# Kernel tuning notes

Hardware: AMD Instinct MI355X
Metric: run time of the kernel (lower is better)

Reference implementation:

```python
import jax, jax.numpy as jnp
import numpy as np

N = 8192
E = 262144
C = 256          # in_channels
OUT = 256        # out_channels
H = 4            # num_heads
DH = C // H      # head dim


def setup_inputs() -> dict:
    key = jax.random.key(0)
    ks = jax.random.split(key, 12)
    stdv = 1.0 / np.sqrt(C)
    inp = {
        "x": jax.random.normal(ks[0], (N, C), dtype=jnp.float32),
        "adj": jax.random.randint(ks[1], (2, E), 0, N, dtype=jnp.int64),
        "weight_local": jax.random.uniform(ks[2], (C, C), jnp.float32, -stdv, stdv),
        # nn.MultiheadAttention packed projections
        "in_proj_w": jax.random.normal(ks[3], (3 * C, C), jnp.float32) * stdv,
        "in_proj_b": jnp.zeros((3 * C,), jnp.float32),
        "out_proj_w": jax.random.normal(ks[4], (C, C), jnp.float32) * stdv,
        "out_proj_b": jnp.zeros((C,), jnp.float32),
        "ln_g": jnp.ones((C,), jnp.float32),
        "ln_b": jnp.zeros((C,), jnp.float32),
        "alpha": jnp.zeros((), jnp.float32),
        "fc_w": jax.random.normal(ks[5], (OUT, C), jnp.float32) * stdv,
        "fc_b": jnp.zeros((OUT,), jnp.float32),
    }
    return inp


def _gcn_conv(x, edge_index):
    # out[col] += (1/sqrt(d[col]*d[row])) * x[row], d = in-degree by col
    row, col = edge_index[0], edge_index[1]
    n = x.shape[0]
    d = jax.ops.segment_sum(jnp.ones((edge_index.shape[1],), x.dtype), col, num_segments=n)
    val = jax.lax.rsqrt(d[col] * d[row])
    val = jnp.where(jnp.isfinite(val), val, 0.0)
    msg = x[row] * val[:, None]                      # [E, C] gather + scale
    return jax.ops.segment_sum(msg, col, num_segments=n)  # [N, C] scatter-add


def _mha(x, in_proj_w, in_proj_b, out_proj_w, out_proj_b):
    # single-batch self-attention over all N nodes
    qkv = x @ in_proj_w.T + in_proj_b                # [N, 3C]
    q, k, v = jnp.split(qkv, 3, axis=-1)
    def heads(t):
        return t.reshape(N, H, DH).transpose(1, 0, 2)  # [H, N, DH]
    q, k, v = heads(q), heads(k), heads(v)
    scores = jnp.einsum("hnd,hmd->hnm", q, k) / np.sqrt(DH)  # [H, N, N]
    attn = jax.nn.softmax(scores, axis=-1)
    out = jnp.einsum("hnm,hmd->hnd", attn, v)        # [H, N, DH]
    out = out.transpose(1, 0, 2).reshape(N, C)
    return out @ out_proj_w.T + out_proj_b


def _layernorm(x, g, b, eps=1e-5):
    mu = jnp.mean(x, axis=-1, keepdims=True)
    var = jnp.var(x, axis=-1, keepdims=True)
    return (x - mu) * jax.lax.rsqrt(var + eps) * g + b


def reference(x, adj, weight_local, in_proj_w, in_proj_b, out_proj_w, out_proj_b,
              ln_g, ln_b, alpha, fc_w, fc_b):
    hi = _gcn_conv(x, adj)
    local_embed = hi @ weight_local                   # [N, C]
    attn_out = _mha(x, in_proj_w, in_proj_b, out_proj_w, out_proj_b)
    global_embed = _layernorm(x + attn_out, ln_g, ln_b)
    w = jax.nn.sigmoid(alpha)
    combined = w * local_embed + (1.0 - w) * global_embed
    return combined @ fc_w.T + fc_b                   # [N, OUT]
```

## Files before the change

kernel.cpp:

```cpp
#include <hip/hip_runtime.h>
#include <hip/hip_bf16.h>
#include <math.h>

#define NN   8192
#define EE   262144
#define CC   256
#define HH   4

typedef __bf16 bf16;
typedef __bf16 bf16x8 __attribute__((ext_vector_type(8)));
typedef __bf16 bf16x4 __attribute__((ext_vector_type(4)));
typedef __bf16 bf16x2 __attribute__((ext_vector_type(2)));
typedef float  f32x4  __attribute__((ext_vector_type(4)));

static __device__ __forceinline__ bf16 f2bf(float f) { return (bf16)f; }

static __device__ __forceinline__ unsigned pk2(float a, float b) {
    __hip_bfloat162 h = __float22bfloat162_rn(float2{a, b});
    return *reinterpret_cast<unsigned*>(&h);
}

__global__ void cvt_f32_bf16(const float* __restrict__ in, bf16* __restrict__ out, int n) {
    for (int i = blockIdx.x * blockDim.x + threadIdx.x; i < n; i += gridDim.x * blockDim.x)
        out[i] = f2bf(in[i]);
}

__global__ void cvt_weights(const float* __restrict__ ipw, const float* __restrict__ opw,
                            const float* __restrict__ fcw, const float* __restrict__ wloc,
                            bf16* __restrict__ ipwb, bf16* __restrict__ opwb,
                            bf16* __restrict__ fcwb, bf16* __restrict__ wlTb) {
    int b = blockIdx.x, t = threadIdx.x;
    if (b < 768)       { int i = b * 256 + t;          ipwb[i] = f2bf(ipw[i]); }
    else if (b < 1024) { int i = (b - 768) * 256 + t;  opwb[i] = f2bf(opw[i]); }
    else if (b < 1280) { int i = (b - 1024) * 256 + t; fcwb[i] = f2bf(fcw[i]); }
    else               { int n = b - 1280;             wlTb[n * 256 + t] = f2bf(wloc[t * 256 + n]); }
}

__global__ __launch_bounds__(256) void build_kpk(const bf16* __restrict__ qkv,
                                                 bf16* __restrict__ Kpk) {
    __shared__ bf16 tl[64][72];
    const int bx = blockIdx.x;
    const int h  = blockIdx.y;
    const int tid = threadIdx.x;
    #pragma unroll
    for (int i = 0; i < 2; i++) {
        int u = tid + i * 256;
        int key = u >> 3, g = u & 7;
        *reinterpret_cast<bf16x8*>(&tl[key][g * 8]) =
            *reinterpret_cast<const bf16x8*>(qkv + (size_t)(bx * 64 + key) * 768 + 256 + h * 64 + g * 8);
    }
    __syncthreads();
    #pragma unroll
    for (int i = 0; i < 2; i++) {
        int ee = tid + i * 256;
        int l15 = ee & 15, quad = (ee >> 4) & 3, c = (ee >> 6) & 1, ktl = ee >> 7;
        int key_local = (ktl >> 1) * 32 + (l15 >> 2) * 8 + (ktl & 1) * 4 + (l15 & 3);
        bf16x8 v = *reinterpret_cast<const bf16x8*>(&tl[key_local][c * 32 + quad * 8]);
        *reinterpret_cast<bf16x8*>(Kpk + ((size_t)((h * 512 + bx * 4 + ktl) * 2 + c)) * 512
                                       + (quad * 16 + l15) * 8) = v;
    }
}

__global__ __launch_bounds__(256) void build_vpk(const bf16* __restrict__ qkv,
                                                 bf16* __restrict__ Vpk) {
    __shared__ bf16 tl[64][72];
    const int bx = blockIdx.x;
    const int h  = blockIdx.y;
    const int tid = threadIdx.x;
    #pragma unroll
    for (int i = 0; i < 2; i++) {
        int u = tid + i * 256;
        int key = u >> 3, g = u & 7;
        *reinterpret_cast<bf16x8*>(&tl[key][g * 8]) =
            *reinterpret_cast<const bf16x8*>(qkv + (size_t)(bx * 64 + key) * 768 + 512 + h * 64 + g * 8);
    }
    __syncthreads();
    #pragma unroll
    for (int i = 0; i < 2; i++) {
        int ee = tid + i * 256;
        int l15 = ee & 15, quad = (ee >> 4) & 3, nt = (ee >> 6) & 3, kcl = ee >> 8;
        bf16x8 v;
        #pragma unroll
        for (int j = 0; j < 8; j++) v[j] = tl[kcl * 32 + quad * 8 + j][nt * 16 + l15];
        *reinterpret_cast<bf16x8*>(Vpk + ((size_t)((h * 256 + bx * 2 + kcl) * 4 + nt)) * 512
                                       + (quad * 16 + l15) * 8) = v;
    }
}

__global__ void degree_i(const int* __restrict__ adj, int* __restrict__ ideg) {
    int e = blockIdx.x * 256 + threadIdx.x;
    if (e < EE) atomicAdd(&ideg[adj[EE + e]], 1);
}

__global__ __launch_bounds__(256) void scan_offsets(const int* __restrict__ ideg,
        int* __restrict__ off, int* __restrict__ cursor, float* __restrict__ rs) {
    __shared__ int ps[256];
    const int tid = threadIdx.x;
    const int base = tid * 32;
    int loc[32];
    int s = 0;
    #pragma unroll
    for (int i = 0; i < 32; i++) { loc[i] = s; s += ideg[base + i]; }
    ps[tid] = s;
    __syncthreads();
    for (int d = 1; d < 256; d <<= 1) {
        int v = (tid >= d) ? ps[tid - d] : 0;
        __syncthreads();
        ps[tid] += v;
        __syncthreads();
    }
    int excl = ps[tid] - s;
    #pragma unroll
    for (int i = 0; i < 32; i++) {
        int o = excl + loc[i];
        off[base + i] = o;
        cursor[base + i] = o;
        int dg = ideg[base + i];
        rs[base + i] = dg > 0 ? rsqrtf((float)dg) : 0.f;
    }
    if (tid == 255) off[8192] = excl + s;
}

__global__ void fill_csr(const int* __restrict__ adj, int* __restrict__ cursor,
                         int* __restrict__ csr) {
    int e = blockIdx.x * 256 + threadIdx.x;
    if (e < EE) {
        int col = adj[EE + e];
        int pos = atomicAdd(&cursor[col], 1);
        csr[pos] = adj[e];
    }
}

__global__ __launch_bounds__(256) void gcn_gather2(const bf16* __restrict__ xb,
        const int* __restrict__ csr, const int* __restrict__ off,
        const float* __restrict__ rs, bf16* __restrict__ hib) {
    const int col = blockIdx.x;
    const int t = threadIdx.x;
    const int half = t >> 7;
    const int j = t & 127;
    const int o = off[col];
    const int cnt = off[col + 1] - o;
    const float rsc = rs[col];
    float a0 = 0.f, a1 = 0.f;
    for (int e = half; e < cnt; e += 2) {
        int r = csr[o + e];
        float v = rsc * rs[r];
        unsigned u = ((const unsigned*)(xb + (size_t)r * CC))[j];
        a0 += __uint_as_float(u << 16) * v;
        a1 += __uint_as_float(u & 0xffff0000u) * v;
    }
    __shared__ float red[512];
    red[half * 256 + 2 * j]     = a0;
    red[half * 256 + 2 * j + 1] = a1;
    __syncthreads();
    if (t < 128) {
        float s0 = red[2 * t]     + red[256 + 2 * t];
        float s1 = red[2 * t + 1] + red[256 + 2 * t + 1];
        bf16x2 pk; pk[0] = f2bf(s0); pk[1] = f2bf(s1);
        ((bf16x2*)(hib + (size_t)col * CC))[t] = pk;
    }
}

__global__ __launch_bounds__(256) void gemm_bt(
        const bf16* __restrict__ A, const bf16* __restrict__ W,
        const float* __restrict__ bias,
        float* __restrict__ outF, bf16* __restrict__ outB,
        int M, int N, int K) {
    const int tid  = threadIdx.x;
    const int wave = tid >> 6;
    const int lane = tid & 63;
    const int quad = lane >> 4;
    const int l15  = lane & 15;
    const int m0 = blockIdx.x * 128;
    const int n0 = blockIdx.y * 64;

    __shared__ bf16 Alds[128][72];
    __shared__ bf16 Wlds[64][72];

    f32x4 acc[2][4];
    #pragma unroll
    for (int mt = 0; mt < 2; mt++)
        #pragma unroll
        for (int nt = 0; nt < 4; nt++)
            acc[mt][nt] = (f32x4){0.f, 0.f, 0.f, 0.f};

    for (int k0 = 0; k0 < K; k0 += 64) {
        #pragma unroll
        for (int i = 0; i < 4; i++) {
            int u = tid + i * 256;
            int r = u >> 3;
            int cp = u & 7;
            *reinterpret_cast<bf16x8*>(&Alds[r][cp * 8]) =
                *reinterpret_cast<const bf16x8*>(A + (size_t)(m0 + r) * K + k0 + cp * 8);
        }
        #pragma unroll
        for (int i = 0; i < 2; i++) {
            int u = tid + i * 256;
            int r = u >> 3;
            int cp = u & 7;
            *reinterpret_cast<bf16x8*>(&Wlds[r][cp * 8]) =
                *reinterpret_cast<const bf16x8*>(W + (size_t)(n0 + r) * K + k0 + cp * 8);
        }
        __syncthreads();
        #pragma unroll
        for (int c = 0; c < 2; c++) {
            bf16x8 af[2], wf[4];
            #pragma unroll
            for (int mt = 0; mt < 2; mt++)
                af[mt] = *reinterpret_cast<const bf16x8*>(&Alds[wave * 32 + mt * 16 + l15][c * 32 + quad * 8]);
            #pragma unroll
            for (int nt = 0; nt < 4; nt++)
                wf[nt] = *reinterpret_cast<const bf16x8*>(&Wlds[nt * 16 + l15][c * 32 + quad * 8]);
            #pragma unroll
            for (int mt = 0; mt < 2; mt++)
                #pragma unroll
                for (int nt = 0; nt < 4; nt++)
                    acc[mt][nt] = __builtin_amdgcn_mfma_f32_16x16x32_bf16(af[mt], wf[nt], acc[mt][nt], 0, 0, 0);
        }
        __syncthreads();
    }
    #pragma unroll
    for (int mt = 0; mt < 2; mt++)
        #pragma unroll
        for (int nt = 0; nt < 4; nt++)
            #pragma unroll
            for (int r = 0; r < 4; r++) {
                int m = m0 + wave * 32 + mt * 16 + quad * 4 + r;
                int n = n0 + nt * 16 + l15;
                float v = acc[mt][nt][r];
                if (bias) v += bias[n];
                if (outF) outF[(size_t)m * N + n] = v;
                else      outB[(size_t)m * N + n] = f2bf(v);
            }
}

__global__ __launch_bounds__(256, 2) void flash_attn6(const bf16* __restrict__ qkv,
                                                      const bf16* __restrict__ Kpk,
                                                      const bf16* __restrict__ Vpk,
                                                      bf16* __restrict__ attnO) {
    const int tid  = threadIdx.x;
    const int w    = tid >> 6;
    const int lane = tid & 63;
    const int quad = lane >> 4;
    const int l15  = lane & 15;
    const int h     = blockIdx.x & 3;
    const int qbase = (blockIdx.x >> 2) * 64;

    __shared__ bf16 Osh[4][64][68];
    __shared__ float lsh[4][64];

    const float qs = 0.180336880f;
    bf16x8 qf[4][2];
    #pragma unroll
    for (int qt = 0; qt < 4; qt++)
        #pragma unroll
        for (int c = 0; c < 2; c++) {
            bf16x8 raw = *reinterpret_cast<const bf16x8*>(
                qkv + (size_t)(qbase + qt * 16 + l15) * 768 + h * 64 + c * 32 + quad * 8);
            #pragma unroll
            for (int j = 0; j < 8; j++) qf[qt][c][j] = f2bf((float)raw[j] * qs);
        }

    const bf16* Kb = Kpk + (size_t)h * 524288 + lane * 8;
    const bf16* Vb = Vpk + (size_t)h * 524288 + lane * 8;

    f32x4 oacc[4][4];
    #pragma unroll
    for (int qt = 0; qt < 4; qt++)
        #pragma unroll
        for (int nt = 0; nt < 4; nt++) oacc[qt][nt] = (f32x4){0.f, 0.f, 0.f, 0.f};
    f32x4 lacc[4];
    #pragma unroll
    for (int qt = 0; qt < 4; qt++) lacc[qt] = (f32x4){0.f, 0.f, 0.f, 0.f};
    bf16x8 onesf;
    #pragma unroll
    for (int j = 0; j < 8; j++) onesf[j] = f2bf(1.0f);
    const f32x4 z4 = (f32x4){0.f, 0.f, 0.f, 0.f};

    bf16x8 kfA[2][2], vfA[4], kfB[2][2], vfB[4];

    #define LOADKV(kc, kf, vf)                                                          \
        {                                                                               \
            _Pragma("unroll")                                                           \
            for (int s = 0; s < 2; s++)                                                 \
                _Pragma("unroll")                                                       \
                for (int c = 0; c < 2; c++)                                             \
                    kf[s][c] = *reinterpret_cast<const bf16x8*>(Kb + (kc) * 2048 + s * 1024 + c * 512); \
            _Pragma("unroll")                                                           \
            for (int nt = 0; nt < 4; nt++)                                              \
                vf[nt] = *reinterpret_cast<const bf16x8*>(Vb + (kc) * 2048 + nt * 512); \
        }

    #define COMPUTE(kf, vf)                                                             \
        {                                                                               \
            f32x4 sacc[2][4];                                                           \
            _Pragma("unroll")                                                           \
            for (int s = 0; s < 2; s++)                                                 \
                _Pragma("unroll")                                                       \
                for (int qt = 0; qt < 4; qt++) {                                        \
                    sacc[s][qt] = __builtin_amdgcn_mfma_f32_16x16x32_bf16(kf[s][0], qf[qt][0], z4, 0, 0, 0); \
                    sacc[s][qt] = __builtin_amdgcn_mfma_f32_16x16x32_bf16(kf[s][1], qf[qt][1], sacc[s][qt], 0, 0, 0); \
                }                                                                       \
            _Pragma("unroll")                                                           \
            for (int qt = 0; qt < 4; qt++) {                                            \
                float e0 = __builtin_amdgcn_exp2f(sacc[0][qt][0]);                      \
                float e1 = __builtin_amdgcn_exp2f(sacc[0][qt][1]);                      \
                float e2 = __builtin_amdgcn_exp2f(sacc[0][qt][2]);                      \
                float e3 = __builtin_amdgcn_exp2f(sacc[0][qt][3]);                      \
                float e4 = __builtin_amdgcn_exp2f(sacc[1][qt][0]);                      \
                float e5 = __builtin_amdgcn_exp2f(sacc[1][qt][1]);                      \
                float e6 = __builtin_amdgcn_exp2f(sacc[1][qt][2]);                      \
                float e7 = __builtin_amdgcn_exp2f(sacc[1][qt][3]);                      \
                union { bf16x8 v; unsigned u[4]; } pu;                                  \
                pu.u[0] = pk2(e0, e1);                                                  \
                pu.u[1] = pk2(e2, e3);                                                  \
                pu.u[2] = pk2(e4, e5);                                                  \
                pu.u[3] = pk2(e6, e7);                                                  \
                _Pragma("unroll")                                                       \
                for (int nt = 0; nt < 4; nt++)                                          \
                    oacc[qt][nt] = __builtin_amdgcn_mfma_f32_16x16x32_bf16(pu.v, vf[nt], oacc[qt][nt], 0, 0, 0); \
                lacc[qt] = __builtin_amdgcn_mfma_f32_16x16x32_bf16(pu.v, onesf, lacc[qt], 0, 0, 0); \
            }                                                                           \
        }

    LOADKV(w, kfA, vfA);
    for (int it = 0; it < 64; it += 2) {
        const int kB = w + (it + 1) * 4;
        LOADKV(kB, kfB, vfB);
        COMPUTE(kfA, vfA);
        int kA2 = w + (it + 2) * 4;
        if (kA2 > 255) kA2 = w;
        LOADKV(kA2, kfA, vfA);
        COMPUTE(kfB, vfB);
    }
    #undef LOADKV
    #undef COMPUTE

    #pragma unroll
    for (int qt = 0; qt < 4; qt++)
        #pragma unroll
        for (int nt = 0; nt < 4; nt++)
            #pragma unroll
            for (int r = 0; r < 4; r++)
                Osh[w][qt * 16 + quad * 4 + r][nt * 16 + l15] = f2bf(oacc[qt][nt][r]);
    if (l15 == 0) {
        #pragma unroll
        for (int qt = 0; qt < 4; qt++)
            #pragma unroll
            for (int r = 0; r < 4; r++)
                lsh[w][qt * 16 + quad * 4 + r] = lacc[qt][r];
    }
    __syncthreads();

    const int q = w * 16 + l15;
    float lstar = lsh[0][q] + lsh[1][q] + lsh[2][q] + lsh[3][q];
    float linv = 1.f / lstar;
    #pragma unroll
    for (int gg = 0; gg < 4; gg++) {
        int d0 = gg * 16 + quad * 4;
        f32x4 acc = (f32x4){0.f, 0.f, 0.f, 0.f};
        #pragma unroll
        for (int v = 0; v < 4; v++) {
            bf16x4 ov = *reinterpret_cast<const bf16x4*>(&Osh[v][q][d0]);
            #pragma unroll
            for (int i = 0; i < 4; i++) acc[i] += (float)ov[i];
        }
        bf16x4 ob;
        #pragma unroll
        for (int i = 0; i < 4; i++) ob[i] = f2bf(acc[i] * linv);
        *reinterpret_cast<bf16x4*>(attnO + (size_t)(qbase + q) * CC + h * 64 + d0) = ob;
    }
}

__global__ __launch_bounds__(256) void ln_combine2(
        const float* __restrict__ x, const float* __restrict__ aproj,
        const float* __restrict__ local, const float* __restrict__ g,
        const float* __restrict__ b, const float* __restrict__ alpha_p,
        bf16* __restrict__ comb) {
    const int row = blockIdx.x * 4 + (threadIdx.x >> 6);
    const int lane = threadIdx.x & 63;
    const f32x4 xv = ((const f32x4*)(x + (size_t)row * CC))[lane];
    const f32x4 av = ((const f32x4*)(aproj + (size_t)row * CC))[lane];
    f32x4 v = xv + av;
    float s = v[0] + v[1] + v[2] + v[3];
    #pragma unroll
    for (int off = 1; off < 64; off <<= 1) s += __shfl_xor(s, off);
    float mu = s * (1.f / CC);
    f32x4 d = v - mu;
    float ss = d[0] * d[0] + d[1] * d[1] + d[2] * d[2] + d[3] * d[3];
    #pragma unroll
    for (int off = 1; off < 64; off <<= 1) ss += __shfl_xor(ss, off);
    float rstd = rsqrtf(ss * (1.f / CC) + 1e-5f);
    const f32x4 gv = ((const f32x4*)g)[lane];
    const f32x4 bv = ((const f32x4*)b)[lane];
    const f32x4 lv = ((const f32x4*)(local + (size_t)row * CC))[lane];
    float wgt = 1.f / (1.f + __expf(-alpha_p[0]));
    bf16x4 o;
    #pragma unroll
    for (int i = 0; i < 4; i++)
        o[i] = f2bf(wgt * lv[i] + (1.f - wgt) * (d[i] * rstd * gv[i] + bv[i]));
    ((bf16x4*)(comb + (size_t)row * CC))[lane] = o;
}

extern "C" void kernel_launch(void* const* d_in, const int* in_sizes, int n_in,
                              void* d_out, int out_size, void* d_ws, size_t ws_size,
                              hipStream_t stream) {
    (void)in_sizes; (void)n_in; (void)out_size; (void)ws_size;
    const float* x    = (const float*)d_in[0];
    const int*   adj  = (const int*)d_in[1];
    const float* wloc = (const float*)d_in[2];
    const float* ipw  = (const float*)d_in[3];
    const float* ipb  = (const float*)d_in[4];
    const float* opw  = (const float*)d_in[5];
    const float* opb  = (const float*)d_in[6];
    const float* lng  = (const float*)d_in[7];
    const float* lnb  = (const float*)d_in[8];
    const float* alp  = (const float*)d_in[9];
    const float* fcw  = (const float*)d_in[10];
    const float* fcb  = (const float*)d_in[11];
    float* out = (float*)d_out;

    char* p = (char*)d_ws;
    int*   ideg   = (int*)p;    p += (size_t)NN * 4;
    int*   off    = (int*)p;    p += (size_t)(NN + 1) * 4;
    int*   cursor = (int*)p;    p += (size_t)NN * 4;
    float* rs     = (float*)p;  p += (size_t)NN * 4;
    int*   csr    = (int*)p;    p += (size_t)EE * 4;
    bf16* xb    = (bf16*)p;   p += (size_t)NN * CC * 2;
    bf16* hib   = (bf16*)p;   p += (size_t)NN * CC * 2;
    bf16* ipwb  = (bf16*)p;   p += (size_t)768 * 256 * 2;
    bf16* wlTb  = (bf16*)p;   p += (size_t)256 * 256 * 2;
    bf16* opwb  = (bf16*)p;   p += (size_t)256 * 256 * 2;
    bf16* fcwb  = (bf16*)p;   p += (size_t)256 * 256 * 2;
    bf16* qkvb  = (bf16*)p;   p += (size_t)NN * 768 * 2;
    bf16* Kpk   = (bf16*)p;   p += (size_t)HH * 512 * 2 * 512 * 2;
    bf16* Vpk   = (bf16*)p;   p += (size_t)HH * 256 * 4 * 512 * 2;
    bf16* aOb   = (bf16*)p;   p += (size_t)NN * CC * 2;
    float* aprj = (float*)p;  p += (size_t)NN * CC * 4;
    float* locl = (float*)p;  p += (size_t)NN * CC * 4;
    bf16* comb  = (bf16*)p;   p += (size_t)NN * CC * 2;

    hipMemsetAsync(ideg, 0, (size_t)NN * 4, stream);

    cvt_f32_bf16<<<2048, 256, 0, stream>>>(x, xb, NN * CC);
    cvt_weights<<<1536, 256, 0, stream>>>(ipw, opw, fcw, wloc, ipwb, opwb, fcwb, wlTb);

    degree_i<<<EE / 256, 256, 0, stream>>>(adj, ideg);
    scan_offsets<<<1, 256, 0, stream>>>(ideg, off, cursor, rs);
    fill_csr<<<EE / 256, 256, 0, stream>>>(adj, cursor, csr);
    gcn_gather2<<<NN, 256, 0, stream>>>(xb, csr, off, rs, hib);

    gemm_bt<<<dim3(NN / 128, 768 / 64), 256, 0, stream>>>(xb, ipwb, ipb, nullptr, qkvb, NN, 768, 256);
    build_kpk<<<dim3(NN / 64, HH), 256, 0, stream>>>(qkvb, Kpk);
    build_vpk<<<dim3(NN / 64, HH), 256, 0, stream>>>(qkvb, Vpk);
    flash_attn6<<<512, 256, 0, stream>>>(qkvb, Kpk, Vpk, aOb);
    gemm_bt<<<dim3(NN / 128, 256 / 64), 256, 0, stream>>>(aOb, opwb, opb, aprj, nullptr, NN, 256, 256);
    gemm_bt<<<dim3(NN / 128, 256 / 64), 256, 0, stream>>>(hib, wlTb, nullptr, locl, nullptr, NN, 256, 256);
    ln_combine2<<<NN / 4, 256, 0, stream>>>(x, aprj, locl, lng, lnb, alp, comb);
    gemm_bt<<<dim3(NN / 128, 256 / 64), 256, 0, stream>>>(comb, fcwb, fcb, out, nullptr, NN, 256, 256);
}
```

Measured before the change: 297.8 us.

## Split attention keys across two blocks, merge partials, and fuse prep kernels

```diff
diff --git a/kernel.cpp b/kernel.cpp
--- a/kernel.cpp
+++ b/kernel.cpp
@@ -20,24 +20,28 @@
     return *reinterpret_cast<unsigned*>(&h);
 }
 
-__global__ void cvt_f32_bf16(const float* __restrict__ in, bf16* __restrict__ out, int n) {
-    for (int i = blockIdx.x * blockDim.x + threadIdx.x; i < n; i += gridDim.x * blockDim.x)
-        out[i] = f2bf(in[i]);
-}
-
-__global__ void cvt_weights(const float* __restrict__ ipw, const float* __restrict__ opw,
-                            const float* __restrict__ fcw, const float* __restrict__ wloc,
-                            bf16* __restrict__ ipwb, bf16* __restrict__ opwb,
-                            bf16* __restrict__ fcwb, bf16* __restrict__ wlTb) {
+__global__ void prep_all(const float* __restrict__ x, bf16* __restrict__ xb,
+                         const float* __restrict__ ipw, const float* __restrict__ opw,
+                         const float* __restrict__ fcw, const float* __restrict__ wloc,
+                         bf16* __restrict__ ipwb, bf16* __restrict__ opwb,
+                         bf16* __restrict__ fcwb, bf16* __restrict__ wlTb,
+                         const int* __restrict__ adj, int* __restrict__ ideg) {
     int b = blockIdx.x, t = threadIdx.x;
-    if (b < 768)       { int i = b * 256 + t;          ipwb[i] = f2bf(ipw[i]); }
-    else if (b < 1024) { int i = (b - 768) * 256 + t;  opwb[i] = f2bf(opw[i]); }
-    else if (b < 1280) { int i = (b - 1024) * 256 + t; fcwb[i] = f2bf(fcw[i]); }
-    else               { int n = b - 1280;             wlTb[n * 256 + t] = f2bf(wloc[t * 256 + n]); }
-}
-
-__global__ __launch_bounds__(256) void build_kpk(const bf16* __restrict__ qkv,
-                                                 bf16* __restrict__ Kpk) {
+    if (b < 2048) {
+        for (int i = b * 256 + t; i < NN * CC; i += 2048 * 256) xb[i] = f2bf(x[i]);
+    } else if (b < 2816) { int i = (b - 2048) * 256 + t; ipwb[i] = f2bf(ipw[i]); }
+    else if (b < 3072)   { int i = (b - 2816) * 256 + t; opwb[i] = f2bf(opw[i]); }
+    else if (b < 3328)   { int i = (b - 3072) * 256 + t; fcwb[i] = f2bf(fcw[i]); }
+    else if (b < 3584)   { int n = b - 3328;             wlTb[n * 256 + t] = f2bf(wloc[t * 256 + n]); }
+    else {
+        int e = (b - 3584) * 256 + t;
+        if (e < EE) atomicAdd(&ideg[adj[EE + e]], 1);
+    }
+}
+
+__global__ __launch_bounds__(256) void build_kv(const bf16* __restrict__ qkv,
+                                                bf16* __restrict__ Kpk,
+                                                bf16* __restrict__ Vpk) {
     __shared__ bf16 tl[64][72];
     const int bx = blockIdx.x;
     const int h  = blockIdx.y;
@@ -59,14 +63,7 @@
         *reinterpret_cast<bf16x8*>(Kpk + ((size_t)((h * 512 + bx * 4 + ktl) * 2 + c)) * 512
                                        + (quad * 16 + l15) * 8) = v;
     }
-}
-
-__global__ __launch_bounds__(256) void build_vpk(const bf16* __restrict__ qkv,
-                                                 bf16* __restrict__ Vpk) {
-    __shared__ bf16 tl[64][72];
-    const int bx = blockIdx.x;
-    const int h  = blockIdx.y;
-    const int tid = threadIdx.x;
+    __syncthreads();
     #pragma unroll
     for (int i = 0; i < 2; i++) {
         int u = tid + i * 256;
@@ -85,11 +82,6 @@
         *reinterpret_cast<bf16x8*>(Vpk + ((size_t)((h * 256 + bx * 2 + kcl) * 4 + nt)) * 512
                                        + (quad * 16 + l15) * 8) = v;
     }
-}
-
-__global__ void degree_i(const int* __restrict__ adj, int* __restrict__ ideg) {
-    int e = blockIdx.x * 256 + threadIdx.x;
-    if (e < EE) atomicAdd(&ideg[adj[EE + e]], 1);
 }
 
 __global__ __launch_bounds__(256) void scan_offsets(const int* __restrict__ ideg,
@@ -234,17 +226,21 @@
             }
 }
 
-__global__ __launch_bounds__(256, 2) void flash_attn6(const bf16* __restrict__ qkv,
+__global__ __launch_bounds__(256, 3) void flash_attn7(const bf16* __restrict__ qkv,
                                                       const bf16* __restrict__ Kpk,
                                                       const bf16* __restrict__ Vpk,
-                                                      bf16* __restrict__ attnO) {
+                                                      bf16* __restrict__ Opart,
+                                                      float* __restrict__ lpart) {
     const int tid  = threadIdx.x;
     const int w    = tid >> 6;
     const int lane = tid & 63;
     const int quad = lane >> 4;
     const int l15  = lane & 15;
-    const int h     = blockIdx.x & 3;
-    const int qbase = (blockIdx.x >> 2) * 64;
+    const int bx = blockIdx.x;
+    const int h    = bx & 3;
+    const int qb   = (bx >> 2) & 127;
+    const int half = bx >> 9;
+    const int qbase = qb * 64;
 
     __shared__ bf16 Osh[4][64][68];
     __shared__ float lsh[4][64];
@@ -263,6 +259,7 @@
 
     const bf16* Kb = Kpk + (size_t)h * 524288 + lane * 8;
     const bf16* Vb = Vpk + (size_t)h * 524288 + lane * 8;
+    const int cbase = half * 128 + w;
 
     f32x4 oacc[4][4];
     #pragma unroll
@@ -277,64 +274,47 @@
     for (int j = 0; j < 8; j++) onesf[j] = f2bf(1.0f);
     const f32x4 z4 = (f32x4){0.f, 0.f, 0.f, 0.f};
 
-    bf16x8 kfA[2][2], vfA[4], kfB[2][2], vfB[4];
-
-    #define LOADKV(kc, kf, vf)                                                          \
-        {                                                                               \
-            _Pragma("unroll")                                                           \
-            for (int s = 0; s < 2; s++)                                                 \
-                _Pragma("unroll")                                                       \
-                for (int c = 0; c < 2; c++)                                             \
-                    kf[s][c] = *reinterpret_cast<const bf16x8*>(Kb + (kc) * 2048 + s * 1024 + c * 512); \
-            _Pragma("unroll")                                                           \
-            for (int nt = 0; nt < 4; nt++)                                              \
-                vf[nt] = *reinterpret_cast<const bf16x8*>(Vb + (kc) * 2048 + nt * 512); \
-        }
-
-    #define COMPUTE(kf, vf)                                                             \
-        {                                                                               \
-            f32x4 sacc[2][4];                                                           \
-            _Pragma("unroll")                                                           \
-            for (int s = 0; s < 2; s++)                                                 \
-                _Pragma("unroll")                                                       \
-                for (int qt = 0; qt < 4; qt++) {                                        \
-                    sacc[s][qt] = __builtin_amdgcn_mfma_f32_16x16x32_bf16(kf[s][0], qf[qt][0], z4, 0, 0, 0); \
-                    sacc[s][qt] = __builtin_amdgcn_mfma_f32_16x16x32_bf16(kf[s][1], qf[qt][1], sacc[s][qt], 0, 0, 0); \
-                }                                                                       \
-            _Pragma("unroll")                                                           \
-            for (int qt = 0; qt < 4; qt++) {                                            \
-                float e0 = __builtin_amdgcn_exp2f(sacc[0][qt][0]);                      \
-                float e1 = __builtin_amdgcn_exp2f(sacc[0][qt][1]);                      \
-                float e2 = __builtin_amdgcn_exp2f(sacc[0][qt][2]);                      \
-                float e3 = __builtin_amdgcn_exp2f(sacc[0][qt][3]);                      \
-                float e4 = __builtin_amdgcn_exp2f(sacc[1][qt][0]);                      \
-                float e5 = __builtin_amdgcn_exp2f(sacc[1][qt][1]);                      \
-                float e6 = __builtin_amdgcn_exp2f(sacc[1][qt][2]);                      \
-                float e7 = __builtin_amdgcn_exp2f(sacc[1][qt][3]);                      \
-                union { bf16x8 v; unsigned u[4]; } pu;                                  \
-                pu.u[0] = pk2(e0, e1);                                                  \
-                pu.u[1] = pk2(e2, e3);                                                  \
-                pu.u[2] = pk2(e4, e5);                                                  \
-                pu.u[3] = pk2(e6, e7);                                                  \
-                _Pragma("unroll")                                                       \
-                for (int nt = 0; nt < 4; nt++)                                          \
-                    oacc[qt][nt] = __builtin_amdgcn_mfma_f32_16x16x32_bf16(pu.v, vf[nt], oacc[qt][nt], 0, 0, 0); \
-                lacc[qt] = __builtin_amdgcn_mfma_f32_16x16x32_bf16(pu.v, onesf, lacc[qt], 0, 0, 0); \
-            }                                                                           \
-        }
-
-    LOADKV(w, kfA, vfA);
-    for (int it = 0; it < 64; it += 2) {
-        const int kB = w + (it + 1) * 4;
-        LOADKV(kB, kfB, vfB);
-        COMPUTE(kfA, vfA);
-        int kA2 = w + (it + 2) * 4;
-        if (kA2 > 255) kA2 = w;
-        LOADKV(kA2, kfA, vfA);
-        COMPUTE(kfB, vfB);
-    }
-    #undef LOADKV
-    #undef COMPUTE
+    for (int i = 0; i < 32; i++) {
+        const int kc = cbase + i * 4;
+        bf16x8 kf[2][2], vf[4];
+        #pragma unroll
+        for (int s = 0; s < 2; s++)
+            #pragma unroll
+            for (int c = 0; c < 2; c++)
+                kf[s][c] = *reinterpret_cast<const bf16x8*>(Kb + kc * 2048 + s * 1024 + c * 512);
+        #pragma unroll
+        for (int nt = 0; nt < 4; nt++)
+            vf[nt] = *reinterpret_cast<const bf16x8*>(Vb + kc * 2048 + nt * 512);
+
+        f32x4 sacc[2][4];
+        #pragma unroll
+        for (int s = 0; s < 2; s++)
+            #pragma unroll
+            for (int qt = 0; qt < 4; qt++) {
+                sacc[s][qt] = __builtin_amdgcn_mfma_f32_16x16x32_bf16(kf[s][0], qf[qt][0], z4, 0, 0, 0);
+                sacc[s][qt] = __builtin_amdgcn_mfma_f32_16x16x32_bf16(kf[s][1], qf[qt][1], sacc[s][qt], 0, 0, 0);
+            }
+        #pragma unroll
+        for (int qt = 0; qt < 4; qt++) {
+            float e0 = __builtin_amdgcn_exp2f(sacc[0][qt][0]);
+            float e1 = __builtin_amdgcn_exp2f(sacc[0][qt][1]);
+            float e2 = __builtin_amdgcn_exp2f(sacc[0][qt][2]);
+            float e3 = __builtin_amdgcn_exp2f(sacc[0][qt][3]);
+            float e4 = __builtin_amdgcn_exp2f(sacc[1][qt][0]);
+            float e5 = __builtin_amdgcn_exp2f(sacc[1][qt][1]);
+            float e6 = __builtin_amdgcn_exp2f(sacc[1][qt][2]);
+            float e7 = __builtin_amdgcn_exp2f(sacc[1][qt][3]);
+            union { bf16x8 v; unsigned u[4]; } pu;
+            pu.u[0] = pk2(e0, e1);
+            pu.u[1] = pk2(e2, e3);
+            pu.u[2] = pk2(e4, e5);
+            pu.u[3] = pk2(e6, e7);
+            #pragma unroll
+            for (int nt = 0; nt < 4; nt++)
+                oacc[qt][nt] = __builtin_amdgcn_mfma_f32_16x16x32_bf16(pu.v, vf[nt], oacc[qt][nt], 0, 0, 0);
+            lacc[qt] = __builtin_amdgcn_mfma_f32_16x16x32_bf16(pu.v, onesf, lacc[qt], 0, 0, 0);
+        }
+    }
 
     #pragma unroll
     for (int qt = 0; qt < 4; qt++)
@@ -353,8 +333,10 @@
     __syncthreads();
 
     const int q = w * 16 + l15;
-    float lstar = lsh[0][q] + lsh[1][q] + lsh[2][q] + lsh[3][q];
-    float linv = 1.f / lstar;
+    const size_t ob = (size_t)half * 2097152 + ((size_t)(h * 128 + qb) * 64 + q) * 64;
+    if (quad == 0)
+        lpart[half * 32768 + (h * 128 + qb) * 64 + q] =
+            lsh[0][q] + lsh[1][q] + lsh[2][q] + lsh[3][q];
     #pragma unroll
     for (int gg = 0; gg < 4; gg++) {
         int d0 = gg * 16 + quad * 4;
@@ -365,11 +347,38 @@
             #pragma unroll
             for (int i = 0; i < 4; i++) acc[i] += (float)ov[i];
         }
-        bf16x4 ob;
-        #pragma unroll
-        for (int i = 0; i < 4; i++) ob[i] = f2bf(acc[i] * linv);
-        *reinterpret_cast<bf16x4*>(attnO + (size_t)(qbase + q) * CC + h * 64 + d0) = ob;
-    }
+        bf16x4 obv;
+        #pragma unroll
+        for (int i = 0; i < 4; i++) obv[i] = f2bf(acc[i]);
+        *reinterpret_cast<bf16x4*>(Opart + ob + d0) = obv;
+    }
+}
+
+__global__ __launch_bounds__(256) void attn_merge(const bf16* __restrict__ Opart,
+                                                  const float* __restrict__ lpart,
+                                                  bf16* __restrict__ attnO) {
+    const int b = blockIdx.x;
+    const int h = b >> 7;
+    const int qb = b & 127;
+    const int t = threadIdx.x;
+    const int q = t >> 2;
+    const int dg = t & 3;
+    const float linv = 1.f / (lpart[b * 64 + q] + lpart[32768 + b * 64 + q]);
+    const bf16* p0 = Opart + ((size_t)b * 64 + q) * 64 + dg * 16;
+    const bf16* p1 = p0 + 2097152;
+    bf16x8 a0 = *reinterpret_cast<const bf16x8*>(p0);
+    bf16x8 a1 = *reinterpret_cast<const bf16x8*>(p0 + 8);
+    bf16x8 b0 = *reinterpret_cast<const bf16x8*>(p1);
+    bf16x8 b1 = *reinterpret_cast<const bf16x8*>(p1 + 8);
+    bf16x8 o0, o1;
+    #pragma unroll
+    for (int i = 0; i < 8; i++) {
+        o0[i] = f2bf(((float)a0[i] + (float)b0[i]) * linv);
+        o1[i] = f2bf(((float)a1[i] + (float)b1[i]) * linv);
+    }
+    bf16* dst = attnO + (size_t)(qb * 64 + q) * CC + h * 64 + dg * 16;
+    *reinterpret_cast<bf16x8*>(dst) = o0;
+    *reinterpret_cast<bf16x8*>(dst + 8) = o1;
 }
 
 __global__ __launch_bounds__(256) void ln_combine2(
@@ -439,21 +448,20 @@
     float* aprj = (float*)p;  p += (size_t)NN * CC * 4;
     float* locl = (float*)p;  p += (size_t)NN * CC * 4;
     bf16* comb  = (bf16*)p;   p += (size_t)NN * CC * 2;
+    bf16*  Opart = (bf16*)aprj;
+    float* lpart = (float*)locl;
 
     hipMemsetAsync(ideg, 0, (size_t)NN * 4, stream);
 
-    cvt_f32_bf16<<<2048, 256, 0, stream>>>(x, xb, NN * CC);
-    cvt_weights<<<1536, 256, 0, stream>>>(ipw, opw, fcw, wloc, ipwb, opwb, fcwb, wlTb);
-
-    degree_i<<<EE / 256, 256, 0, stream>>>(adj, ideg);
+    prep_all<<<4608, 256, 0, stream>>>(x, xb, ipw, opw, fcw, wloc, ipwb, opwb, fcwb, wlTb, adj, ideg);
     scan_offsets<<<1, 256, 0, stream>>>(ideg, off, cursor, rs);
     fill_csr<<<EE / 256, 256, 0, stream>>>(adj, cursor, csr);
     gcn_gather2<<<NN, 256, 0, stream>>>(xb, csr, off, rs, hib);
 
     gemm_bt<<<dim3(NN / 128, 768 / 64), 256, 0, stream>>>(xb, ipwb, ipb, nullptr, qkvb, NN, 768, 256);
-    build_kpk<<<dim3(NN / 64, HH), 256, 0, stream>>>(qkvb, Kpk);
-    build_vpk<<<dim3(NN / 64, HH), 256, 0, stream>>>(qkvb, Vpk);
-    flash_attn6<<<512, 256, 0, stream>>>(qkvb, Kpk, Vpk, aOb);
+    build_kv<<<dim3(NN / 64, HH), 256, 0, stream>>>(qkvb, Kpk, Vpk);
+    flash_attn7<<<1024, 256, 0, stream>>>(qkvb, Kpk, Vpk, Opart, lpart);
+    attn_merge<<<512, 256, 0, stream>>>(Opart, lpart, aOb);
     gemm_bt<<<dim3(NN / 128, 256 / 64), 256, 0, stream>>>(aOb, opwb, opb, aprj, nullptr, NN, 256, 256);
     gemm_bt<<<dim3(NN / 128, 256 / 64), 256, 0, stream>>>(hib, wlTb, nullptr, locl, nullptr, NN, 256, 256);
     ln_combine2<<<NN / 4, 256, 0, stream>>>(x, aprj, locl, lng, lnb, alp, comb);
```

Result: slower. 310.0 us (+4.1%).

## Fuse prep and K/V packing kernels, merge GEMMs, widen flash-attention blocks

Applied to the files above, without the earlier changes.

```diff
diff --git a/kernel.cpp b/kernel.cpp
--- a/kernel.cpp
+++ b/kernel.cpp
@@ -20,24 +20,28 @@
     return *reinterpret_cast<unsigned*>(&h);
 }
 
-__global__ void cvt_f32_bf16(const float* __restrict__ in, bf16* __restrict__ out, int n) {
-    for (int i = blockIdx.x * blockDim.x + threadIdx.x; i < n; i += gridDim.x * blockDim.x)
-        out[i] = f2bf(in[i]);
-}
-
-__global__ void cvt_weights(const float* __restrict__ ipw, const float* __restrict__ opw,
-                            const float* __restrict__ fcw, const float* __restrict__ wloc,
-                            bf16* __restrict__ ipwb, bf16* __restrict__ opwb,
-                            bf16* __restrict__ fcwb, bf16* __restrict__ wlTb) {
+__global__ void prep_all(const float* __restrict__ x, bf16* __restrict__ xb,
+                         const float* __restrict__ ipw, const float* __restrict__ opw,
+                         const float* __restrict__ fcw, const float* __restrict__ wloc,
+                         bf16* __restrict__ ipwb, bf16* __restrict__ opwb,
+                         bf16* __restrict__ fcwb, bf16* __restrict__ wlTb,
+                         const int* __restrict__ adj, int* __restrict__ ideg) {
     int b = blockIdx.x, t = threadIdx.x;
-    if (b < 768)       { int i = b * 256 + t;          ipwb[i] = f2bf(ipw[i]); }
-    else if (b < 1024) { int i = (b - 768) * 256 + t;  opwb[i] = f2bf(opw[i]); }
-    else if (b < 1280) { int i = (b - 1024) * 256 + t; fcwb[i] = f2bf(fcw[i]); }
-    else               { int n = b - 1280;             wlTb[n * 256 + t] = f2bf(wloc[t * 256 + n]); }
-}
-
-__global__ __launch_bounds__(256) void build_kpk(const bf16* __restrict__ qkv,
-                                                 bf16* __restrict__ Kpk) {
+    if (b < 2048) {
+        for (int i = b * 256 + t; i < NN * CC; i += 2048 * 256) xb[i] = f2bf(x[i]);
+    } else if (b < 2816) { int i = (b - 2048) * 256 + t; ipwb[i] = f2bf(ipw[i]); }
+    else if (b < 3072)   { int i = (b - 2816) * 256 + t; opwb[i] = f2bf(opw[i]); }
+    else if (b < 3328)   { int i = (b - 3072) * 256 + t; fcwb[i] = f2bf(fcw[i]); }
+    else if (b < 3584)   { int n = b - 3328;             wlTb[n * 256 + t] = f2bf(wloc[t * 256 + n]); }
+    else {
+        int e = (b - 3584) * 256 + t;
+        if (e < EE) atomicAdd(&ideg[adj[EE + e]], 1);
+    }
+}
+
+__global__ __launch_bounds__(256) void build_kv(const bf16* __restrict__ qkv,
+                                                bf16* __restrict__ Kpk,
+                                                bf16* __restrict__ Vpk) {
     __shared__ bf16 tl[64][72];
     const int bx = blockIdx.x;
     const int h  = blockIdx.y;
@@ -59,14 +63,7 @@
         *reinterpret_cast<bf16x8*>(Kpk + ((size_t)((h * 512 + bx * 4 + ktl) * 2 + c)) * 512
                                        + (quad * 16 + l15) * 8) = v;
     }
-}
-
-__global__ __launch_bounds__(256) void build_vpk(const bf16* __restrict__ qkv,
-                                                 bf16* __restrict__ Vpk) {
-    __shared__ bf16 tl[64][72];
-    const int bx = blockIdx.x;
-    const int h  = blockIdx.y;
-    const int tid = threadIdx.x;
+    __syncthreads();
     #pragma unroll
     for (int i = 0; i < 2; i++) {
         int u = tid + i * 256;
@@ -85,11 +82,6 @@
         *reinterpret_cast<bf16x8*>(Vpk + ((size_t)((h * 256 + bx * 2 + kcl) * 4 + nt)) * 512
                                        + (quad * 16 + l15) * 8) = v;
     }
-}
-
-__global__ void degree_i(const int* __restrict__ adj, int* __restrict__ ideg) {
-    int e = blockIdx.x * 256 + threadIdx.x;
-    if (e < EE) atomicAdd(&ideg[adj[EE + e]], 1);
 }
 
 __global__ __launch_bounds__(256) void scan_offsets(const int* __restrict__ ideg,
@@ -161,11 +153,11 @@
     }
 }
 
-__global__ __launch_bounds__(256) void gemm_bt(
+static __device__ __forceinline__ void gemm_core(
         const bf16* __restrict__ A, const bf16* __restrict__ W,
         const float* __restrict__ bias,
         float* __restrict__ outF, bf16* __restrict__ outB,
-        int M, int N, int K) {
+        int M, int N, int K, bf16 (*Alds)[72], bf16 (*Wlds)[72]) {
     const int tid  = threadIdx.x;
     const int wave = tid >> 6;
     const int lane = tid & 63;
@@ -173,9 +165,6 @@
     const int l15  = lane & 15;
     const int m0 = blockIdx.x * 128;
     const int n0 = blockIdx.y * 64;
-
-    __shared__ bf16 Alds[128][72];
-    __shared__ bf16 Wlds[64][72];
 
     f32x4 acc[2][4];
     #pragma unroll
@@ -234,20 +223,45 @@
             }
 }
 
-__global__ __launch_bounds__(256, 2) void flash_attn6(const bf16* __restrict__ qkv,
-                                                      const bf16* __restrict__ Kpk,
-                                                      const bf16* __restrict__ Vpk,
-                                                      bf16* __restrict__ attnO) {
+__global__ __launch_bounds__(256) void gemm_bt(
+        const bf16* __restrict__ A, const bf16* __restrict__ W,
+        const float* __restrict__ bias,
+        float* __restrict__ outF, bf16* __restrict__ outB,
+        int M, int N, int K) {
+    __shared__ bf16 Alds[128][72];
+    __shared__ bf16 Wlds[64][72];
+    gemm_core(A, W, bias, outF, outB, M, N, K, Alds, Wlds);
+}
+
+__global__ __launch_bounds__(256) void gemm_dual(
+        const bf16* __restrict__ A0, const bf16* __restrict__ W0,
+        const float* __restrict__ b0, float* __restrict__ o0,
+        const bf16* __restrict__ A1, const bf16* __restrict__ W1,
+        float* __restrict__ o1) {
+    __shared__ bf16 Alds[128][72];
+    __shared__ bf16 Wlds[64][72];
+    if (blockIdx.z == 0) gemm_core(A0, W0, b0, o0, nullptr, NN, 256, 256, Alds, Wlds);
+    else                 gemm_core(A1, W1, nullptr, o1, nullptr, NN, 256, 256, Alds, Wlds);
+}
+
+__global__ __launch_bounds__(512, 2) void flash_attn10(const bf16* __restrict__ qkv,
+                                                       const bf16* __restrict__ Kpk,
+                                                       const bf16* __restrict__ Vpk,
+                                                       bf16* __restrict__ attnO) {
     const int tid  = threadIdx.x;
     const int w    = tid >> 6;
+    const int g    = w >> 2;
+    const int k4   = w & 3;
     const int lane = tid & 63;
     const int quad = lane >> 4;
     const int l15  = lane & 15;
-    const int h     = blockIdx.x & 3;
-    const int qbase = (blockIdx.x >> 2) * 64;
-
-    __shared__ bf16 Osh[4][64][68];
-    __shared__ float lsh[4][64];
+    const int bx = blockIdx.x;
+    const int h  = bx & 3;
+    const int qb = bx >> 2;
+    const int qbase = qb * 128 + g * 64;
+
+    __shared__ bf16 Osh[8][64][68];
+    __shared__ float lsh[8][64];
 
     const float qs = 0.180336880f;
     bf16x8 qf[4][2];
@@ -323,13 +337,13 @@
             }                                                                           \
         }
 
-    LOADKV(w, kfA, vfA);
+    LOADKV(k4, kfA, vfA);
     for (int it = 0; it < 64; it += 2) {
-        const int kB = w + (it + 1) * 4;
+        const int kB = k4 + (it + 1) * 4;
         LOADKV(kB, kfB, vfB);
         COMPUTE(kfA, vfA);
-        int kA2 = w + (it + 2) * 4;
-        if (kA2 > 255) kA2 = w;
+        int kA2 = k4 + (it + 2) * 4;
+        if (kA2 > 255) kA2 = k4;
         LOADKV(kA2, kfA, vfA);
         COMPUTE(kfB, vfB);
     }
@@ -352,24 +366,32 @@
     }
     __syncthreads();
 
-    const int q = w * 16 + l15;
-    float lstar = lsh[0][q] + lsh[1][q] + lsh[2][q] + lsh[3][q];
-    float linv = 1.f / lstar;
-    #pragma unroll
-    for (int gg = 0; gg < 4; gg++) {
-        int d0 = gg * 16 + quad * 4;
-        f32x4 acc = (f32x4){0.f, 0.f, 0.f, 0.f};
-        #pragma unroll
-        for (int v = 0; v < 4; v++) {
-            bf16x4 ov = *reinterpret_cast<const bf16x4*>(&Osh[v][q][d0]);
-            #pragma unroll
-            for (int i = 0; i < 4; i++) acc[i] += (float)ov[i];
-        }
-        bf16x4 ob;
-        #pragma unroll
-        for (int i = 0; i < 4; i++) ob[i] = f2bf(acc[i] * linv);
-        *reinterpret_cast<bf16x4*>(attnO + (size_t)(qbase + q) * CC + h * 64 + d0) = ob;
-    }
+    const int q7 = tid >> 2;
+    const int gg = q7 >> 6;
+    const int ql = q7 & 63;
+    const int ds = (tid & 3) * 16;
+    const int wb = gg * 4;
+    float lsum = lsh[wb][ql] + lsh[wb + 1][ql] + lsh[wb + 2][ql] + lsh[wb + 3][ql];
+    float linv = 1.f / lsum;
+    float acc[16];
+    #pragma unroll
+    for (int i = 0; i < 16; i++) acc[i] = 0.f;
+    #pragma unroll
+    for (int v = 0; v < 4; v++) {
+        bf16x8 o0 = *reinterpret_cast<const bf16x8*>(&Osh[wb + v][ql][ds]);
+        bf16x8 o1 = *reinterpret_cast<const bf16x8*>(&Osh[wb + v][ql][ds + 8]);
+        #pragma unroll
+        for (int i = 0; i < 8; i++) { acc[i] += (float)o0[i]; acc[8 + i] += (float)o1[i]; }
+    }
+    bf16x8 ob0, ob1;
+    #pragma unroll
+    for (int i = 0; i < 8; i++) {
+        ob0[i] = f2bf(acc[i] * linv);
+        ob1[i] = f2bf(acc[8 + i] * linv);
+    }
+    bf16* dst = attnO + (size_t)(qb * 128 + q7) * CC + h * 64 + ds;
+    *reinterpret_cast<bf16x8*>(dst) = ob0;
+    *reinterpret_cast<bf16x8*>(dst + 8) = ob1;
 }
 
 __global__ __launch_bounds__(256) void ln_combine2(
@@ -442,20 +464,15 @@
 
     hipMemsetAsync(ideg, 0, (size_t)NN * 4, stream);
 
-    cvt_f32_bf16<<<2048, 256, 0, stream>>>(x, xb, NN * CC);
-    cvt_weights<<<1536, 256, 0, stream>>>(ipw, opw, fcw, wloc, ipwb, opwb, fcwb, wlTb);
-
-    degree_i<<<EE / 256, 256, 0, stream>>>(adj, ideg);
+    prep_all<<<4608, 256, 0, stream>>>(x, xb, ipw, opw, fcw, wloc, ipwb, opwb, fcwb, wlTb, adj, ideg);
     scan_offsets<<<1, 256, 0, stream>>>(ideg, off, cursor, rs);
     fill_csr<<<EE / 256, 256, 0, stream>>>(adj, cursor, csr);
     gcn_gather2<<<NN, 256, 0, stream>>>(xb, csr, off, rs, hib);
 
     gemm_bt<<<dim3(NN / 128, 768 / 64), 256, 0, stream>>>(xb, ipwb, ipb, nullptr, qkvb, NN, 768, 256);
-    build_kpk<<<dim3(NN / 64, HH), 256, 0, stream>>>(qkvb, Kpk);
-    build_vpk<<<dim3(NN / 64, HH), 256, 0, stream>>>(qkvb, Vpk);
-    flash_attn6<<<512, 256, 0, stream>>>(qkvb, Kpk, Vpk, aOb);
-    gemm_bt<<<dim3(NN / 128, 256 / 64), 256, 0, stream>>>(aOb, opwb, opb, aprj, nullptr, NN, 256, 256);
-    gemm_bt<<<dim3(NN / 128, 256 / 64), 256, 0, stream>>>(hib, wlTb, nullptr, locl, nullptr, NN, 256, 256);
+    build_kv<<<dim3(NN / 64, HH), 256, 0, stream>>>(qkvb, Kpk, Vpk);
+    flash_attn10<<<256, 512, 0, stream>>>(qkvb, Kpk, Vpk, aOb);
+    gemm_dual<<<dim3(NN / 128, 4, 2), 256, 0, stream>>>(aOb, opwb, opb, aprj, hib, wlTb, locl);
     ln_combine2<<<NN / 4, 256, 0, stream>>>(x, aprj, locl, lng, lnb, alp, comb);
     gemm_bt<<<dim3(NN / 128, 256 / 64), 256, 0, stream>>>(comb, fcwb, fcb, out, nullptr, NN, 256, 256);
 }
```

Result: faster. 283.0 us (-5.0%).
